# Kernel optimization log

Measured on AMD Instinct MI355X. Metric: run time of the kernel, lower is better.

The kernel has to match this reference:

```python
import jax, jax.numpy as jnp
import numpy as np

L = 8            # gat_blocks(4) * layers(2)
LAYERS = 2
RC, DC, SC, EC = 32, 32, 256, 512
IN_DIM, OUT_DIM = 2, 12
N_NODES, EMB, D_ATT = 512, 16, 16
B, T_IN = 8, 13  # T_IN == receptive_field -> no left padding


def setup_inputs() -> dict:
    key = jax.random.key(0)
    ks = jax.random.split(key, 12)
    g = lambda k, shp: jax.random.normal(k, shp, jnp.float32) * 0.05
    return {
        "input": jax.random.normal(ks[0], (B, IN_DIM, N_NODES, T_IN), jnp.float32),
        "gat_supports": jax.random.normal(ks[1], (EMB, N_NODES), jnp.float32),
        "start_w": g(ks[2], (RC, IN_DIM)), "start_b": jnp.zeros((RC,), jnp.float32),
        "filt_w": g(ks[3], (L, DC, RC, 1, 2)), "filt_b": jnp.zeros((L, DC), jnp.float32),
        "gate_w": g(ks[4], (L, DC, RC, 1, 2)), "gate_b": jnp.zeros((L, DC), jnp.float32),
        "skip_w": g(ks[5], (L, SC, DC)), "skip_b": jnp.zeros((L, SC), jnp.float32),
        "q_w": g(ks[6], (L, D_ATT, DC + EMB)), "q_b": jnp.zeros((L, D_ATT), jnp.float32),
        "k_w": g(ks[7], (L, D_ATT, DC + EMB)), "k_b": jnp.zeros((L, D_ATT), jnp.float32),
        "gmlp_w": g(ks[8], (L, RC, 2 * DC)), "gmlp_b": jnp.zeros((L, RC), jnp.float32),
        "bn_g": jnp.ones((L, RC), jnp.float32), "bn_b": jnp.zeros((L, RC), jnp.float32),
        "end1_w": g(ks[9], (EC, SC)), "end1_b": jnp.zeros((EC,), jnp.float32),
        "end2_w": g(ks[10], (OUT_DIM, EC)), "end2_b": jnp.zeros((OUT_DIM,), jnp.float32),
    }


def _pw(x, w, b):
    # 1x1 conv (pointwise linear over channels): x [B,C,N,T], w [O,C]
    return jnp.einsum('oc,bcnt->bont', w, x) + b[None, :, None, None]


def _tconv(x, w, b, d):
    # dilated temporal conv, kernel (1,2), VALID (shrinks T by d)
    y = jax.lax.conv_general_dilated(
        x, w, window_strides=(1, 1), padding='VALID', rhs_dilation=(1, d),
        dimension_numbers=('NCHW', 'OIHW', 'NCHW'))
    return y + b[None, :, None, None]


def _bn(x, g, b, eps=1e-5):
    # BatchNorm2d (training-mode batch stats, biased variance, as in torch)
    m = jnp.mean(x, axis=(0, 2, 3), keepdims=True)
    v = jnp.var(x, axis=(0, 2, 3), keepdims=True)
    return g[None, :, None, None] * (x - m) * jax.lax.rsqrt(v + eps) + b[None, :, None, None]


def _forward(input, gat_supports, start_w, start_b, filt_w, filt_b, gate_w, gate_b,
             skip_w, skip_b, q_w, q_b, k_w, k_b, gmlp_w, gmlp_b, bn_g, bn_b,
             end1_w, end1_b, end2_w, end2_b):
    x = _pw(input, start_w, start_b)          # [B,RC,N,T]
    skip = None
    scale = 1.0 / (D_ATT ** 0.5)
    for i in range(L):
        d = 2 ** (i % LAYERS)                 # dilation schedule 1,2 per block
        residual = x
        f = jnp.tanh(_tconv(residual, filt_w[i], filt_b[i], d))
        gt = jax.nn.sigmoid(_tconv(residual, gate_w[i], gate_b[i], d))
        x = f * gt                            # [B,DC,N,T-d]
        s = _pw(x, skip_w[i], skip_b[i])      # [B,SC,N,T-d]
        skip = s if skip is None else s + skip[:, :, :, -s.shape[3]:]
        # --- adaptive graph attention ---
        Bn, C, N, T = x.shape
        emb = jnp.broadcast_to(gat_supports[None, :, :, None], (Bn, EMB, N, T))
        xe = jnp.concatenate([x, emb], axis=1)            # [B,C+EMB,N,T]
        q = _pw(xe, q_w[i], q_b[i]).transpose(0, 3, 2, 1)  # [B,T,N,d]
        kk = _pw(xe, k_w[i], k_b[i]).transpose(0, 3, 2, 1)
        att = jax.nn.softmax(jnp.einsum('btnd,btmd->btnm', q, kk) * scale, axis=-1)
        xa = jnp.einsum('bcvt,btvw->bcwt', x, att)         # x @ att on node axis
        x = _pw(jnp.concatenate([x, xa], axis=1), gmlp_w[i], gmlp_b[i])
        # ---------------------------------
        x = x + residual[:, :, :, -x.shape[3]:]
        x = _bn(x, bn_g[i], bn_b[i])
    out = jax.nn.relu(skip)
    out = jax.nn.relu(_pw(out, end1_w, end1_b))
    out = _pw(out, end2_w, end2_b)            # [B,OUT_DIM,N,1]
    return out


def reference(input, gat_supports, start_w, start_b, filt_w, filt_b, gate_w, gate_b,
              skip_w, skip_b, q_w, q_b, k_w, k_b, gmlp_w, gmlp_b, bn_g, bn_b,
              end1_w, end1_b, end2_w, end2_b):
    return _forward(input, gat_supports, start_w, start_b, filt_w, filt_b, gate_w,
                    gate_b, skip_w, skip_b, q_w, q_b, k_w, k_b, gmlp_w, gmlp_b,
                    bn_g, bn_b, end1_w, end1_b, end2_w, end2_b)
```

## Files before the change

kernel.cpp:

```cpp
#include <hip/hip_runtime.h>
#include <math.h>


typedef short v4s __attribute__((ext_vector_type(4)));
typedef float v4f __attribute__((ext_vector_type(4)));
typedef unsigned short ushort_t;

#define MFMA16(a,b,c) __builtin_amdgcn_mfma_f32_16x16x16bf16_1k(a, b, c, 0, 0, 0)

__device__ inline ushort_t f2bf(float f){
    unsigned int u = __builtin_bit_cast(unsigned int, f);
    u += 0x7FFFu + ((u >> 16) & 1u);
    return (ushort_t)(u >> 16);
}
__device__ inline float bf2f(ushort_t h){
    return __builtin_bit_cast(float, ((unsigned int)h) << 16);
}

__global__ void k_init_norm(float* normP){
    int t = threadIdx.x;
    normP[t] = (t < 32) ? 1.0f : 0.0f;
}

__global__ void k_emb(const float* __restrict__ qw, const float* __restrict__ qb,
                      const float* __restrict__ kw, const float* __restrict__ kb,
                      const float* __restrict__ gat, float* __restrict__ qe, float* __restrict__ ke){
    int idx = blockIdx.x*256 + threadIdx.x;
    const int total = 8*512*16;
    if (idx >= 2*total) return;
    bool isK = idx >= total;
    int id = isK ? idx - total : idx;
    int dq = id & 15; int n = (id >> 4) & 511; int l = id >> 13;
    const float* w = isK ? kw : qw;
    const float* bi = isK ? kb : qb;
    float acc = bi[l*16 + dq];
    const float* wrow = w + (l*16 + dq)*48 + 32;
    #pragma unroll
    for (int e = 0; e < 16; e++) acc += wrow[e] * gat[e*512 + n];
    (isK ? ke : qe)[(l*512 + n)*16 + dq] = isK ? acc : acc*0.25f;
}

__global__ void k_start(const float* __restrict__ inp, const float* __restrict__ sw,
                        const float* __restrict__ sb, float* __restrict__ x0){
    int idx = blockIdx.x*256 + threadIdx.x;
    if (idx >= 8*13*32*512) return;
    int n = idx & 511; int c = (idx >> 9) & 31; int r = idx >> 14;
    int t = r % 13; int b = r / 13;
    float v0 = inp[((b*2 + 0)*512 + n)*13 + t];
    float v1 = inp[((b*2 + 1)*512 + n)*13 + t];
    x0[idx] = sb[c] + sw[c*2 + 0]*v0 + sw[c*2 + 1]*v1;
}

__global__ void k_wprep(const float* __restrict__ filt_w, const float* __restrict__ gate_w,
                        const float* __restrict__ q_w, const float* __restrict__ k_w,
                        const float* __restrict__ skip_w,
                        ushort_t* __restrict__ cwh, ushort_t* __restrict__ cwl,
                        ushort_t* __restrict__ qkw,
                        ushort_t* __restrict__ swh, ushort_t* __restrict__ swl)
{
    int idx = blockIdx.x*256 + threadIdx.x;
    if (idx < 32768){
        int k = idx & 63, o = (idx >> 6) & 63, l = idx >> 12;
        int c = k & 31, tap = k >> 5;
        float w = (o < 32) ? filt_w[((l*32 + o)*32 + c)*2 + tap]
                           : gate_w[((l*32 + (o-32))*32 + c)*2 + tap];
        ushort_t hi = f2bf(w);
        cwh[idx] = hi; cwl[idx] = f2bf(w - bf2f(hi));
    } else if (idx < 32768 + 8192){
        int j2 = idx - 32768;
        int c = j2 & 31, j = (j2 >> 5) & 31, l = j2 >> 10;
        float w = (j < 16) ? q_w[(l*16 + j)*48 + c]*0.25f : k_w[(l*16 + (j-16))*48 + c];
        qkw[j2] = f2bf(w);
    } else if (idx < 32768 + 8192 + 65536){
        int s = idx - 40960;
        float w = skip_w[s];
        ushort_t hi = f2bf(w);
        swh[s] = hi; swl[s] = f2bf(w - bf2f(hi));
    }
}

__global__ __launch_bounds__(256) void k_gated_mfma(
    const float* __restrict__ xin, int Tin, int d, int Tout,
    const float* __restrict__ normP,
    const ushort_t* __restrict__ cwh, const ushort_t* __restrict__ cwl,
    const float* __restrict__ fb, const float* __restrict__ gb,
    const ushort_t* __restrict__ qkw,
    const float* __restrict__ qe, const float* __restrict__ ke,
    const ushort_t* __restrict__ swh, const ushort_t* __restrict__ swl,
    const float* __restrict__ sb,
    float* __restrict__ skip,
    ushort_t* __restrict__ xbfT, ushort_t* __restrict__ qbf, ushort_t* __restrict__ kbf,
    int do_qk)
{
    __shared__ unsigned int XBP[64*129];
    int tid = threadIdx.x;
    int nch = blockIdx.x, t = blockIdx.y, b = blockIdx.z;
    size_t bt = (size_t)(b*Tout + t);
    int n0 = nch*128;
    int lane = tid & 63, wid = tid >> 6;
    int m16 = lane & 15, g4 = (lane >> 4)*4;

    #pragma unroll
    for (int kk = 0; kk < 16; kk++){
        int k = wid*16 + kk;
        int c = k & 31, tap = k >> 5;
        const float* src = xin + ((size_t)(b*Tin + t + tap*d)*32 + c)*512 + n0 + lane;
        float An = normP[c], Bn = normP[32 + c];
        #pragma unroll
        for (int h = 0; h < 2; h++){
            float xn = An*src[h*64] + Bn;
            ushort_t hi = f2bf(xn);
            ushort_t lo = f2bf(xn - bf2f(hi));
            XBP[k*129 + h*64 + lane] = (unsigned int)hi | ((unsigned int)lo << 16);
        }
    }
    v4s ah[4][4], al[4][4];
    #pragma unroll
    for (int ot = 0; ot < 4; ot++)
    #pragma unroll
    for (int kt = 0; kt < 4; kt++){
        ah[ot][kt] = *(const v4s*)(cwh + (ot*16 + m16)*64 + kt*16 + g4);
        al[ot][kt] = *(const v4s*)(cwl + (ot*16 + m16)*64 + kt*16 + g4);
    }
    v4f acc[4][2];
    #pragma unroll
    for (int ot = 0; ot < 4; ot++){
        float4 bv = *(const float4*)((ot < 2 ? fb + ot*16 : gb + (ot-2)*16) + g4);
        acc[ot][0] = (v4f){bv.x, bv.y, bv.z, bv.w};
        acc[ot][1] = (v4f){bv.x, bv.y, bv.z, bv.w};
    }
    __syncthreads();
    v4s bh[2][4], bl[2][4];
    #pragma unroll
    for (int nt = 0; nt < 2; nt++){
        int nl = (wid*2 + nt)*16 + m16;
        #pragma unroll
        for (int kt = 0; kt < 4; kt++){
            unsigned int u0 = XBP[(kt*16 + g4 + 0)*129 + nl];
            unsigned int u1 = XBP[(kt*16 + g4 + 1)*129 + nl];
            unsigned int u2 = XBP[(kt*16 + g4 + 2)*129 + nl];
            unsigned int u3 = XBP[(kt*16 + g4 + 3)*129 + nl];
            v4s hh, ll;
            hh[0] = (short)(u0 & 0xffffu); ll[0] = (short)(u0 >> 16);
            hh[1] = (short)(u1 & 0xffffu); ll[1] = (short)(u1 >> 16);
            hh[2] = (short)(u2 & 0xffffu); ll[2] = (short)(u2 >> 16);
            hh[3] = (short)(u3 & 0xffffu); ll[3] = (short)(u3 >> 16);
            bh[nt][kt] = hh; bl[nt][kt] = ll;
        }
    }
    #pragma unroll
    for (int kt = 0; kt < 4; kt++)
    #pragma unroll
    for (int ot = 0; ot < 4; ot++)
    #pragma unroll
    for (int nt = 0; nt < 2; nt++){
        acc[ot][nt] = MFMA16(ah[ot][kt], bh[nt][kt], acc[ot][nt]);
        acc[ot][nt] = MFMA16(ah[ot][kt], bl[nt][kt], acc[ot][nt]);
        acc[ot][nt] = MFMA16(al[ot][kt], bh[nt][kt], acc[ot][nt]);
    }
    v4s xh[2][2], xl[2][2];
    #pragma unroll
    for (int ct = 0; ct < 2; ct++)
    #pragma unroll
    for (int nt = 0; nt < 2; nt++){
        v4s hh, ll;
        #pragma unroll
        for (int i = 0; i < 4; i++){
            float f = acc[ct][nt][i], g = acc[ct+2][nt][i];
            float e2 = __expf(2.0f*f);
            float th = 1.0f - 2.0f/(e2 + 1.0f);
            float sg = 1.0f/(1.0f + __expf(-g));
            float v = th*sg;
            ushort_t hi = f2bf(v);
            hh[i] = (short)hi; ll[i] = (short)f2bf(v - bf2f(hi));
        }
        xh[ct][nt] = hh; xl[ct][nt] = ll;
    }
    if (do_qk){
        #pragma unroll
        for (int ct = 0; ct < 2; ct++)
        #pragma unroll
        for (int nt = 0; nt < 2; nt++){
            int nl = n0 + (wid*2 + nt)*16 + m16;
            #pragma unroll
            for (int i = 0; i < 4; i++)
                xbfT[(bt*32 + ct*16 + g4 + i)*512 + nl] = (ushort_t)xh[ct][nt][i];
        }
        v4s qa[2][2];
        #pragma unroll
        for (int ot = 0; ot < 2; ot++)
        #pragma unroll
        for (int kt = 0; kt < 2; kt++)
            qa[ot][kt] = *(const v4s*)(qkw + (ot*16 + m16)*32 + kt*16 + g4);
        #pragma unroll
        for (int ot = 0; ot < 2; ot++)
        #pragma unroll
        for (int nt = 0; nt < 2; nt++){
            int nl = n0 + (wid*2 + nt)*16 + m16;
            float4 ev = *(const float4*)((ot == 0 ? qe : ke) + nl*16 + g4);
            v4f a2 = (v4f){ev.x, ev.y, ev.z, ev.w};
            #pragma unroll
            for (int kt = 0; kt < 2; kt++)
                a2 = MFMA16(qa[ot][kt], xh[kt][nt], a2);
            v4s r;
            #pragma unroll
            for (int i = 0; i < 4; i++) r[i] = (short)f2bf(a2[i]);
            *(v4s*)((ot == 0 ? qbf : kbf) + (bt*512 + nl)*16 + g4) = r;
        }
    }
    if (t == Tout - 1){
        #pragma unroll 4
        for (int ot = 0; ot < 16; ot++){
            v4s sh_[2], sl_[2];
            #pragma unroll
            for (int kt = 0; kt < 2; kt++){
                sh_[kt] = *(const v4s*)(swh + (ot*16 + m16)*32 + kt*16 + g4);
                sl_[kt] = *(const v4s*)(swl + (ot*16 + m16)*32 + kt*16 + g4);
            }
            float4 sbv = *(const float4*)(sb + ot*16 + g4);
            #pragma unroll
            for (int nt = 0; nt < 2; nt++){
                int nl = n0 + (wid*2 + nt)*16 + m16;
                float* sp = skip + ((size_t)(b*512) + nl)*256 + ot*16 + g4;
                float4 old = *(const float4*)sp;
                v4f a3 = (v4f){old.x + sbv.x, old.y + sbv.y, old.z + sbv.z, old.w + sbv.w};
                #pragma unroll
                for (int kt = 0; kt < 2; kt++){
                    a3 = MFMA16(sh_[kt], xh[kt][nt], a3);
                    a3 = MFMA16(sh_[kt], xl[kt][nt], a3);
                    a3 = MFMA16(sl_[kt], xh[kt][nt], a3);
                }
                *(float4*)sp = make_float4(a3[0], a3[1], a3[2], a3[3]);
            }
        }
    }
}

__global__ __launch_bounds__(256) void k_z(
    const ushort_t* __restrict__ qbf, const ushort_t* __restrict__ kbf,
    int Tout, float* __restrict__ rz)
{
    __shared__ ushort_t KS[512*20];
    int tid = threadIdx.x;
    int vchunk = blockIdx.x, t = blockIdx.y, b = blockIdx.z;
    size_t bt = (size_t)(b*Tout + t);
    const ushort_t* kg = kbf + bt*8192;
    const ushort_t* qg = qbf + bt*8192;
    {
        const uint2* s0 = (const uint2*)(kg + tid*16);
        uint2* d0 = (uint2*)(KS + tid*20);
        d0[0]=s0[0]; d0[1]=s0[1]; d0[2]=s0[2]; d0[3]=s0[3];
        const uint2* s1 = (const uint2*)(kg + (tid+256)*16);
        uint2* d1 = (uint2*)(KS + (tid+256)*20);
        d1[0]=s1[0]; d1[1]=s1[1]; d1[2]=s1[2]; d1[3]=s1[3];
    }
    int l = tid & 63, wid = tid >> 6;
    int m16 = l & 15, g4 = (l >> 4)*4;
    __syncthreads();
    #pragma unroll
    for (int vi = 0; vi < 2; vi++){
        int vt = vchunk*8 + wid*2 + vi;
        v4s bq = *(const v4s*)(qg + (vt*16 + m16)*16 + g4);
        float zp = 0.f;
        for (int wt = 0; wt < 32; wt++){
            v4s ak = *(const v4s*)(KS + (wt*16 + m16)*20 + g4);
            v4f s = MFMA16(ak, bq, ((v4f){0.f,0.f,0.f,0.f}));
            zp += __expf(fminf(s[0],60.f)) + __expf(fminf(s[1],60.f))
                + __expf(fminf(s[2],60.f)) + __expf(fminf(s[3],60.f));
        }
        zp += __shfl_xor(zp, 16);
        zp += __shfl_xor(zp, 32);
        if (l < 16) rz[bt*512 + vt*16 + l] = 1.0f/zp;
    }
}

__global__ __launch_bounds__(256) void k_pv(
    const ushort_t* __restrict__ qbf, const ushort_t* __restrict__ kbf,
    const ushort_t* __restrict__ xbfT, const float* __restrict__ rz,
    const float* __restrict__ xin, int Tin, int d, int Tout,
    const float* __restrict__ normP,
    const float* __restrict__ gw, const float* __restrict__ gb,
    float* __restrict__ y, float* __restrict__ bnpart)
{
    __shared__ ushort_t QS[512*20];
    __shared__ ushort_t XT[32*520];
    __shared__ float rzs[512];
    __shared__ float bnsh[256];
    int tid = threadIdx.x;
    int wc = blockIdx.x, t = blockIdx.y, b = blockIdx.z;
    size_t bt = (size_t)(b*Tout + t);
    const ushort_t* qg = qbf + bt*8192;
    const ushort_t* kg = kbf + bt*8192;
    {
        const uint2* s0 = (const uint2*)(qg + tid*16);
        uint2* d0 = (uint2*)(QS + tid*20);
        d0[0]=s0[0]; d0[1]=s0[1]; d0[2]=s0[2]; d0[3]=s0[3];
        const uint2* s1 = (const uint2*)(qg + (tid+256)*16);
        uint2* d1 = (uint2*)(QS + (tid+256)*20);
        d1[0]=s1[0]; d1[1]=s1[1]; d1[2]=s1[2]; d1[3]=s1[3];
        int c = tid >> 3, seg = tid & 7;
        const uint4* xs = (const uint4*)(xbfT + bt*16384 + c*512 + seg*64);
        uint4* xd = (uint4*)(XT + c*520 + seg*64);
        #pragma unroll
        for (int j = 0; j < 8; j++) xd[j] = xs[j];
        rzs[tid] = rz[bt*512 + tid];
        rzs[tid + 256] = rz[bt*512 + tid + 256];
    }
    int l = tid & 63, wid = tid >> 6;
    int m16 = l & 15, g4 = (l >> 4)*4;
    v4s AG[2][2][2];
    #pragma unroll
    for (int pt = 0; pt < 2; pt++)
    #pragma unroll
    for (int ot = 0; ot < 2; ot++)
    #pragma unroll
    for (int ct = 0; ct < 2; ct++){
        float4 gv = *(const float4*)(gw + (ot*16 + m16)*64 + pt*32 + ct*16 + g4);
        v4s r; r[0] = (short)f2bf(gv.x); r[1] = (short)f2bf(gv.y);
        r[2] = (short)f2bf(gv.z); r[3] = (short)f2bf(gv.w);
        AG[pt][ot][ct] = r;
    }
    v4f gbv[2], An[2], Bn[2];
    #pragma unroll
    for (int ot = 0; ot < 2; ot++){
        gbv[ot] = *(const v4f*)(gb + ot*16 + g4);
        An[ot]  = *(const v4f*)(normP + ot*16 + g4);
        Bn[ot]  = *(const v4f*)(normP + 32 + ot*16 + g4);
    }
    int wt0 = wc*8 + wid*2;
    v4s bk[2];
    bk[0] = *(const v4s*)(kg + (wt0*16 + m16)*16 + g4);
    bk[1] = *(const v4s*)(kg + ((wt0+1)*16 + m16)*16 + g4);
    __syncthreads();
    v4f c2[2][2];
    #pragma unroll
    for (int i = 0; i < 2; i++){ c2[i][0] = (v4f){0.f,0.f,0.f,0.f}; c2[i][1] = (v4f){0.f,0.f,0.f,0.f}; }
    for (int vt = 0; vt < 32; vt++){
        v4s aq = *(const v4s*)(QS + (vt*16 + m16)*20 + g4);
        v4f s0 = MFMA16(aq, bk[0], ((v4f){0.f,0.f,0.f,0.f}));
        v4f s1 = MFMA16(aq, bk[1], ((v4f){0.f,0.f,0.f,0.f}));
        v4f rzv = *(const v4f*)(rzs + vt*16 + g4);
        v4s p0, p1;
        #pragma unroll
        for (int i = 0; i < 4; i++){
            p0[i] = (short)f2bf(__expf(fminf(s0[i],60.f)) * rzv[i]);
            p1[i] = (short)f2bf(__expf(fminf(s1[i],60.f)) * rzv[i]);
        }
        #pragma unroll
        for (int ct = 0; ct < 2; ct++){
            v4s ax = *(const v4s*)(XT + (ct*16 + m16)*520 + vt*16 + g4);
            c2[0][ct] = MFMA16(ax, p0, c2[0][ct]);
            c2[1][ct] = MFMA16(ax, p1, c2[1][ct]);
        }
    }
    float bs1[2][4], bs2[2][4];
    #pragma unroll
    for (int ot = 0; ot < 2; ot++)
    #pragma unroll
    for (int i = 0; i < 4; i++){ bs1[ot][i] = 0.f; bs2[ot][i] = 0.f; }
    #pragma unroll
    for (int wtl = 0; wtl < 2; wtl++){
        int wt = wt0 + wtl;
        v4s bxa[2], bx[2];
        #pragma unroll
        for (int ct = 0; ct < 2; ct++){
            v4s r;
            #pragma unroll
            for (int i = 0; i < 4; i++) r[i] = (short)f2bf(c2[wtl][ct][i]);
            bxa[ct] = r;
            v4s q;
            #pragma unroll
            for (int i = 0; i < 4; i++) q[i] = (short)XT[(ct*16 + g4 + i)*520 + wt*16 + m16];
            bx[ct] = q;
        }
        v4f c3[2];
        #pragma unroll
        for (int ot = 0; ot < 2; ot++){
            c3[ot] = gbv[ot];
            #pragma unroll
            for (int ct = 0; ct < 2; ct++){
                c3[ot] = MFMA16(AG[1][ot][ct], bxa[ct], c3[ot]);
                c3[ot] = MFMA16(AG[0][ot][ct], bx[ct],  c3[ot]);
            }
        }
        int wg = wt*16 + m16;
        const float* resbase = xin + ((size_t)(b*Tin + t + d)*32)*512 + wg;
        float* ybase = y + (bt*32)*512 + wg;
        #pragma unroll
        for (int ot = 0; ot < 2; ot++){
            #pragma unroll
            for (int i = 0; i < 4; i++){
                int outc = ot*16 + g4 + i;
                float yv = c3[ot][i] + An[ot][i]*resbase[(size_t)outc*512] + Bn[ot][i];
                ybase[(size_t)outc*512] = yv;
                bs1[ot][i] += yv; bs2[ot][i] += yv*yv;
            }
        }
    }
    #pragma unroll
    for (int off = 1; off <= 8; off <<= 1){
        #pragma unroll
        for (int ot = 0; ot < 2; ot++)
        #pragma unroll
        for (int i = 0; i < 4; i++){
            bs1[ot][i] += __shfl_xor(bs1[ot][i], off);
            bs2[ot][i] += __shfl_xor(bs2[ot][i], off);
        }
    }
    if (m16 == 0){
        #pragma unroll
        for (int ot = 0; ot < 2; ot++)
        #pragma unroll
        for (int i = 0; i < 4; i++){
            int c = ot*16 + g4 + i;
            bnsh[(wid*32 + c)*2 + 0] = bs1[ot][i];
            bnsh[(wid*32 + c)*2 + 1] = bs2[ot][i];
        }
    }
    __syncthreads();
    if (tid < 64){
        int c = tid & 31, p = tid >> 5;
        float s = 0.f;
        #pragma unroll
        for (int w = 0; w < 4; w++) s += bnsh[(w*32 + c)*2 + p];
        bnpart[(bt*4 + wc)*64 + c*2 + p] = s;
    }
}

__global__ __launch_bounds__(1024) void k_bn_fin(
    const float* __restrict__ bnpart, int nparts,
    const float* __restrict__ g, const float* __restrict__ bb,
    float* __restrict__ normPout)
{
    __shared__ float sh[17][64];
    int tid = threadIdx.x;
    int lane = tid & 63, grp = tid >> 6;
    float s = 0.f;
    for (int i = grp; i < nparts; i += 16) s += bnpart[(size_t)i*64 + lane];
    sh[grp][lane] = s;
    __syncthreads();
    if (tid < 64){
        float tot = 0.f;
        #pragma unroll
        for (int gg = 0; gg < 16; gg++) tot += sh[gg][lane];
        sh[16][lane] = tot;
    }
    __syncthreads();
    if (tid < 32){
        float S  = sh[16][tid*2 + 0];
        float S2 = sh[16][tid*2 + 1];
        float cnt = (float)nparts * 128.0f;
        float m = S/cnt;
        float var = S2/cnt - m*m;
        float A = g[tid]*rsqrtf(var + 1e-5f);
        normPout[tid] = A;
        normPout[32 + tid] = bb[tid] - m*A;
    }
}

__global__ void k_split_skip(const float* __restrict__ skip,
                             ushort_t* __restrict__ shi, ushort_t* __restrict__ slo){
    int idx = blockIdx.x*256 + threadIdx.x;
    float v = fmaxf(skip[idx], 0.f);
    ushort_t h = f2bf(v);
    shi[idx] = h; slo[idx] = f2bf(v - bf2f(h));
}

__global__ void k_w1split(const float* __restrict__ w,
                          ushort_t* __restrict__ hi, ushort_t* __restrict__ lo){
    int idx = blockIdx.x*256 + threadIdx.x;
    float v = w[idx];
    ushort_t h = f2bf(v);
    hi[idx] = h; lo[idx] = f2bf(v - bf2f(h));
}

__global__ __launch_bounds__(256) void k_end_h(
    const ushort_t* __restrict__ shi, const ushort_t* __restrict__ slo,
    const ushort_t* __restrict__ w1hi, const ushort_t* __restrict__ w1lo,
    const float* __restrict__ b1, float* __restrict__ h)
{
    __shared__ ushort_t SH[16*264], SL[16*264];
    int tid = threadIdx.x;
    int nc = blockIdx.x, b = blockIdx.y;
    int n0 = nc*16;
    {
        int n = tid >> 4, s = tid & 15;
        const uint4* src = (const uint4*)(shi + ((size_t)(b*512 + n0 + n))*256 + s*16);
        uint4* dst = (uint4*)(SH + n*264 + s*16);
        dst[0] = src[0]; dst[1] = src[1];
        const uint4* src2 = (const uint4*)(slo + ((size_t)(b*512 + n0 + n))*256 + s*16);
        uint4* dst2 = (uint4*)(SL + n*264 + s*16);
        dst2[0] = src2[0]; dst2[1] = src2[1];
    }
    __syncthreads();
    int l = tid & 63, wid = tid >> 6;
    int m16 = l & 15, g4 = (l >> 4)*4;
    v4f acc[8];
    #pragma unroll
    for (int nt = 0; nt < 8; nt++){
        float bo = b1[(wid*8 + nt)*16 + m16];
        acc[nt] = (v4f){bo, bo, bo, bo};
    }
    for (int kk = 0; kk < 16; kk++){
        v4s ahi = *(const v4s*)(SH + m16*264 + kk*16 + g4);
        v4s alo = *(const v4s*)(SL + m16*264 + kk*16 + g4);
        #pragma unroll
        for (int nt = 0; nt < 8; nt++){
            int o = (wid*8 + nt)*16 + m16;
            v4s bhi = *(const v4s*)(w1hi + o*256 + kk*16 + g4);
            v4s blo = *(const v4s*)(w1lo + o*256 + kk*16 + g4);
            acc[nt] = MFMA16(ahi, bhi, acc[nt]);
            acc[nt] = MFMA16(ahi, blo, acc[nt]);
            acc[nt] = MFMA16(alo, bhi, acc[nt]);
        }
    }
    #pragma unroll
    for (int nt = 0; nt < 8; nt++){
        int o = (wid*8 + nt)*16 + m16;
        float4 hv;
        hv.x = fmaxf(acc[nt][0], 0.f);
        hv.y = fmaxf(acc[nt][1], 0.f);
        hv.z = fmaxf(acc[nt][2], 0.f);
        hv.w = fmaxf(acc[nt][3], 0.f);
        *(float4*)(h + ((size_t)(b*512 + o))*512 + n0 + g4) = hv;
    }
}

__global__ __launch_bounds__(64) void k_end2(
    const float* __restrict__ h, const float* __restrict__ w2, const float* __restrict__ b2,
    float* __restrict__ out)
{
    int l = threadIdx.x;
    int nc = blockIdx.x, b = blockIdx.y;
    int n = nc*16 + (l & 15);
    int grp = l >> 4;
    float a0 = b2[grp], a1 = b2[grp+4], a2 = b2[grp+8];
    const float* hb = h + ((size_t)b*512)*512 + n;
    const float* w0 = w2 + (size_t)grp*512;
    const float* w4 = w2 + (size_t)(grp+4)*512;
    const float* w8 = w2 + (size_t)(grp+8)*512;
    for (int o = 0; o < 512; o++){
        float hv = hb[(size_t)o*512];
        a0 += w0[o]*hv; a1 += w4[o]*hv; a2 += w8[o]*hv;
    }
    out[((size_t)b*12 + grp)*512 + n] = a0;
    out[((size_t)b*12 + grp+4)*512 + n] = a1;
    out[((size_t)b*12 + grp+8)*512 + n] = a2;
}

extern "C" void kernel_launch(void* const* d_in, const int* in_sizes, int n_in,
                              void* d_out, int out_size, void* d_ws, size_t ws_size,
                              hipStream_t stream)
{
    (void)in_sizes; (void)n_in; (void)out_size; (void)ws_size;
    const float* input  = (const float*)d_in[0];
    const float* gat    = (const float*)d_in[1];
    const float* start_w= (const float*)d_in[2];
    const float* start_b= (const float*)d_in[3];
    const float* filt_w = (const float*)d_in[4];
    const float* filt_b = (const float*)d_in[5];
    const float* gate_w = (const float*)d_in[6];
    const float* gate_b = (const float*)d_in[7];
    const float* skip_w = (const float*)d_in[8];
    const float* skip_b = (const float*)d_in[9];
    const float* q_w    = (const float*)d_in[10];
    const float* q_b    = (const float*)d_in[11];
    const float* k_w    = (const float*)d_in[12];
    const float* k_b    = (const float*)d_in[13];
    const float* gmlp_w = (const float*)d_in[14];
    const float* gmlp_b = (const float*)d_in[15];
    const float* bn_g   = (const float*)d_in[16];
    const float* bn_b   = (const float*)d_in[17];
    const float* end1_w = (const float*)d_in[18];
    const float* end1_b = (const float*)d_in[19];
    const float* end2_w = (const float*)d_in[20];
    const float* end2_b = (const float*)d_in[21];
    float* out = (float*)d_out;

    float* W = (float*)d_ws;
    size_t off = 0;
    float* bufA = W + off; off += (size_t)8*13*32*512;
    float* bufB = W + off; off += (size_t)8*13*32*512;
    float* skip = W + off; off += (size_t)8*512*256;
    float* qe   = W + off; off += (size_t)8*512*16;
    float* ke   = W + off; off += (size_t)8*512*16;
    float* normP= W + off; off += (size_t)9*64;
    float* bnpart = W + off; off += (size_t)96*4*64;
    float* rz   = W + off; off += (size_t)8*12*512;
    float* h    = W + off; off += (size_t)8*512*512;
    ushort_t* xbfT = (ushort_t*)(W + off); off += (size_t)8*12*32*512/2;
    ushort_t* qbf  = (ushort_t*)(W + off); off += (size_t)8*12*512*16/2;
    ushort_t* kbf  = (ushort_t*)(W + off); off += (size_t)8*12*512*16/2;
    ushort_t* shi  = (ushort_t*)(W + off); off += (size_t)8*512*256/2;
    ushort_t* slo  = (ushort_t*)(W + off); off += (size_t)8*512*256/2;
    ushort_t* w1hi = (ushort_t*)(W + off); off += (size_t)512*256/2;
    ushort_t* w1lo = (ushort_t*)(W + off); off += (size_t)512*256/2;
    ushort_t* cwh  = (ushort_t*)(W + off); off += (size_t)32768/2;
    ushort_t* cwl  = (ushort_t*)(W + off); off += (size_t)32768/2;
    ushort_t* qkw  = (ushort_t*)(W + off); off += (size_t)8192/2;
    ushort_t* swbh = (ushort_t*)(W + off); off += (size_t)65536/2;
    ushort_t* swbl = (ushort_t*)(W + off); off += (size_t)65536/2;

    hipMemsetAsync(skip, 0, (size_t)8*512*256*sizeof(float), stream);
    k_init_norm<<<1, 64, 0, stream>>>(normP);
    k_emb<<<512, 256, 0, stream>>>(q_w, q_b, k_w, k_b, gat, qe, ke);
    k_start<<<6656, 256, 0, stream>>>(input, start_w, start_b, bufA);
    k_w1split<<<512, 256, 0, stream>>>(end1_w, w1hi, w1lo);
    k_wprep<<<416, 256, 0, stream>>>(filt_w, gate_w, q_w, k_w, skip_w, cwh, cwl, qkw, swbh, swbl);

    const int Tin[8] = {13,12,10,9,7,6,4,3};
    const int Dd[8]  = {1,2,1,2,1,2,1,2};
    float* xin = bufA; float* yb = bufB;
    for (int i = 0; i < 8; i++){
        int Ti = Tin[i], d = Dd[i], To = Ti - d;
        k_gated_mfma<<<dim3(4, To, 8), 256, 0, stream>>>(xin, Ti, d, To, normP + i*64,
            cwh + i*4096, cwl + i*4096, filt_b + i*32, gate_b + i*32,
            qkw + i*1024, qe + i*8192, ke + i*8192,
            swbh + i*8192, swbl + i*8192, skip_b + i*256,
            skip, xbfT, qbf, kbf, (i < 7) ? 1 : 0);
        if (i < 7){
            k_z<<<dim3(4, To, 8), 256, 0, stream>>>(qbf, kbf, To, rz);
            k_pv<<<dim3(4, To, 8), 256, 0, stream>>>(qbf, kbf, xbfT, rz,
                xin, Ti, d, To, normP + i*64, gmlp_w + i*2048, gmlp_b + i*32, yb, bnpart);
            k_bn_fin<<<1, 1024, 0, stream>>>(bnpart, 8*To*4, bn_g + i*32, bn_b + i*32, normP + (i+1)*64);
            float* tmp = xin; xin = yb; yb = tmp;
        }
    }
    k_split_skip<<<4096, 256, 0, stream>>>(skip, shi, slo);
    k_end_h<<<dim3(32, 8), 256, 0, stream>>>(shi, slo, w1hi, w1lo, end1_b, h);
    k_end2<<<dim3(32, 8), 64, 0, stream>>>(h, end2_w, end2_b, out);
}
```

Baseline: 501.1 us.

## Fold BN finalize into consumers via atomics and fuse end layers into one kernel

Drops the separate batch-norm finalize kernel: k_pv now atomically accumulates per-channel sums, and the next-layer kernels turn them into scale and shift themselves. Fuses skip ReLU and bf16 splitting, end1 and end2 into a single kernel, with end2 done on MFMA using LDS-resident hidden activations. Also merges the end1 and end2 weight prep into k_wprep and removes the init-norm launch. This cuts kernel launches and the global round trips for h, shi and slo, at the cost of atomic contention and a non-deterministic summation order for the BN statistics.

```diff
diff --git a/kernel.cpp b/kernel.cpp
--- a/kernel.cpp
+++ b/kernel.cpp
@@ -15,11 +15,6 @@
 }
 __device__ inline float bf2f(ushort_t h){
     return __builtin_bit_cast(float, ((unsigned int)h) << 16);
-}
-
-__global__ void k_init_norm(float* normP){
-    int t = threadIdx.x;
-    normP[t] = (t < 32) ? 1.0f : 0.0f;
 }
 
 __global__ void k_emb(const float* __restrict__ qw, const float* __restrict__ qb,
@@ -54,9 +49,12 @@
 __global__ void k_wprep(const float* __restrict__ filt_w, const float* __restrict__ gate_w,
                         const float* __restrict__ q_w, const float* __restrict__ k_w,
                         const float* __restrict__ skip_w,
+                        const float* __restrict__ w1, const float* __restrict__ w2,
                         ushort_t* __restrict__ cwh, ushort_t* __restrict__ cwl,
                         ushort_t* __restrict__ qkw,
-                        ushort_t* __restrict__ swh, ushort_t* __restrict__ swl)
+                        ushort_t* __restrict__ swh, ushort_t* __restrict__ swl,
+                        ushort_t* __restrict__ w1h, ushort_t* __restrict__ w1l,
+                        ushort_t* __restrict__ w2h, ushort_t* __restrict__ w2l)
 {
     int idx = blockIdx.x*256 + threadIdx.x;
     if (idx < 32768){
@@ -66,22 +64,34 @@
                            : gate_w[((l*32 + (o-32))*32 + c)*2 + tap];
         ushort_t hi = f2bf(w);
         cwh[idx] = hi; cwl[idx] = f2bf(w - bf2f(hi));
-    } else if (idx < 32768 + 8192){
+    } else if (idx < 40960){
         int j2 = idx - 32768;
         int c = j2 & 31, j = (j2 >> 5) & 31, l = j2 >> 10;
         float w = (j < 16) ? q_w[(l*16 + j)*48 + c]*0.25f : k_w[(l*16 + (j-16))*48 + c];
         qkw[j2] = f2bf(w);
-    } else if (idx < 32768 + 8192 + 65536){
+    } else if (idx < 106496){
         int s = idx - 40960;
         float w = skip_w[s];
         ushort_t hi = f2bf(w);
         swh[s] = hi; swl[s] = f2bf(w - bf2f(hi));
+    } else if (idx < 237568){
+        int s = idx - 106496;
+        float w = w1[s];
+        ushort_t hi = f2bf(w);
+        w1h[s] = hi; w1l[s] = f2bf(w - bf2f(hi));
+    } else if (idx < 245760){
+        int s = idx - 237568;
+        int od = s >> 9, k = s & 511;
+        float w = (od < 12) ? w2[od*512 + k] : 0.0f;
+        ushort_t hi = f2bf(w);
+        w2h[s] = hi; w2l[s] = f2bf(w - bf2f(hi));
     }
 }
 
 __global__ __launch_bounds__(256) void k_gated_mfma(
     const float* __restrict__ xin, int Tin, int d, int Tout,
-    const float* __restrict__ normP,
+    const float* __restrict__ bnsumP, const float* __restrict__ bnG,
+    const float* __restrict__ bnB, int ident, float cnt,
     const ushort_t* __restrict__ cwh, const ushort_t* __restrict__ cwl,
     const float* __restrict__ fb, const float* __restrict__ gb,
     const ushort_t* __restrict__ qkw,
@@ -93,6 +103,7 @@
     int do_qk)
 {
     __shared__ unsigned int XBP[64*129];
+    __shared__ float ABsh[64];
     int tid = threadIdx.x;
     int nch = blockIdx.x, t = blockIdx.y, b = blockIdx.z;
     size_t bt = (size_t)(b*Tout + t);
@@ -100,12 +111,25 @@
     int lane = tid & 63, wid = tid >> 6;
     int m16 = lane & 15, g4 = (lane >> 4)*4;
 
+    if (tid < 32){
+        float A, Bc;
+        if (ident){ A = 1.0f; Bc = 0.0f; }
+        else {
+            float S = bnsumP[2*tid], S2 = bnsumP[2*tid + 1];
+            float m = S/cnt, var = S2/cnt - m*m;
+            A = bnG[tid]*rsqrtf(var + 1e-5f);
+            Bc = bnB[tid] - m*A;
+        }
+        ABsh[tid] = A; ABsh[32 + tid] = Bc;
+    }
+    __syncthreads();
+
     #pragma unroll
     for (int kk = 0; kk < 16; kk++){
         int k = wid*16 + kk;
         int c = k & 31, tap = k >> 5;
         const float* src = xin + ((size_t)(b*Tin + t + tap*d)*32 + c)*512 + n0 + lane;
-        float An = normP[c], Bn = normP[32 + c];
+        float An = ABsh[c], Bn = ABsh[32 + c];
         #pragma unroll
         for (int h = 0; h < 2; h++){
             float xn = An*src[h*64] + Bn;
@@ -278,14 +302,16 @@
     const ushort_t* __restrict__ qbf, const ushort_t* __restrict__ kbf,
     const ushort_t* __restrict__ xbfT, const float* __restrict__ rz,
     const float* __restrict__ xin, int Tin, int d, int Tout,
-    const float* __restrict__ normP,
+    const float* __restrict__ bnsumP, const float* __restrict__ bnG,
+    const float* __restrict__ bnB, int ident, float cnt,
     const float* __restrict__ gw, const float* __restrict__ gb,
-    float* __restrict__ y, float* __restrict__ bnpart)
+    float* __restrict__ y, float* __restrict__ bnsumOut)
 {
     __shared__ ushort_t QS[512*20];
     __shared__ ushort_t XT[32*520];
     __shared__ float rzs[512];
     __shared__ float bnsh[256];
+    __shared__ float ABsh[64];
     int tid = threadIdx.x;
     int wc = blockIdx.x, t = blockIdx.y, b = blockIdx.z;
     size_t bt = (size_t)(b*Tout + t);
@@ -306,6 +332,17 @@
         rzs[tid] = rz[bt*512 + tid];
         rzs[tid + 256] = rz[bt*512 + tid + 256];
     }
+    if (tid < 32){
+        float A, Bc;
+        if (ident){ A = 1.0f; Bc = 0.0f; }
+        else {
+            float S = bnsumP[2*tid], S2 = bnsumP[2*tid + 1];
+            float m = S/cnt, var = S2/cnt - m*m;
+            A = bnG[tid]*rsqrtf(var + 1e-5f);
+            Bc = bnB[tid] - m*A;
+        }
+        ABsh[tid] = A; ABsh[32 + tid] = Bc;
+    }
     int l = tid & 63, wid = tid >> 6;
     int m16 = l & 15, g4 = (l >> 4)*4;
     v4s AG[2][2][2];
@@ -320,18 +357,23 @@
         r[2] = (short)f2bf(gv.z); r[3] = (short)f2bf(gv.w);
         AG[pt][ot][ct] = r;
     }
-    v4f gbv[2], An[2], Bn[2];
-    #pragma unroll
-    for (int ot = 0; ot < 2; ot++){
-        gbv[ot] = *(const v4f*)(gb + ot*16 + g4);
-        An[ot]  = *(const v4f*)(normP + ot*16 + g4);
-        Bn[ot]  = *(const v4f*)(normP + 32 + ot*16 + g4);
-    }
+    v4f gbv[2];
+    #pragma unroll
+    for (int ot = 0; ot < 2; ot++) gbv[ot] = *(const v4f*)(gb + ot*16 + g4);
     int wt0 = wc*8 + wid*2;
     v4s bk[2];
     bk[0] = *(const v4s*)(kg + (wt0*16 + m16)*16 + g4);
     bk[1] = *(const v4s*)(kg + ((wt0+1)*16 + m16)*16 + g4);
     __syncthreads();
+    v4f An[2], Bn[2];
+    #pragma unroll
+    for (int ot = 0; ot < 2; ot++){
+        #pragma unroll
+        for (int i = 0; i < 4; i++){
+            An[ot][i] = ABsh[ot*16 + g4 + i];
+            Bn[ot][i] = ABsh[32 + ot*16 + g4 + i];
+        }
+    }
     v4f c2[2][2];
     #pragma unroll
     for (int i = 0; i < 2; i++){ c2[i][0] = (v4f){0.f,0.f,0.f,0.f}; c2[i][1] = (v4f){0.f,0.f,0.f,0.f}; }
@@ -423,74 +465,37 @@
         float s = 0.f;
         #pragma unroll
         for (int w = 0; w < 4; w++) s += bnsh[(w*32 + c)*2 + p];
-        bnpart[(bt*4 + wc)*64 + c*2 + p] = s;
-    }
-}
-
-__global__ __launch_bounds__(1024) void k_bn_fin(
-    const float* __restrict__ bnpart, int nparts,
-    const float* __restrict__ g, const float* __restrict__ bb,
-    float* __restrict__ normPout)
-{
-    __shared__ float sh[17][64];
-    int tid = threadIdx.x;
-    int lane = tid & 63, grp = tid >> 6;
-    float s = 0.f;
-    for (int i = grp; i < nparts; i += 16) s += bnpart[(size_t)i*64 + lane];
-    sh[grp][lane] = s;
-    __syncthreads();
-    if (tid < 64){
-        float tot = 0.f;
-        #pragma unroll
-        for (int gg = 0; gg < 16; gg++) tot += sh[gg][lane];
-        sh[16][lane] = tot;
-    }
-    __syncthreads();
-    if (tid < 32){
-        float S  = sh[16][tid*2 + 0];
-        float S2 = sh[16][tid*2 + 1];
-        float cnt = (float)nparts * 128.0f;
-        float m = S/cnt;
-        float var = S2/cnt - m*m;
-        float A = g[tid]*rsqrtf(var + 1e-5f);
-        normPout[tid] = A;
-        normPout[32 + tid] = bb[tid] - m*A;
-    }
-}
-
-__global__ void k_split_skip(const float* __restrict__ skip,
-                             ushort_t* __restrict__ shi, ushort_t* __restrict__ slo){
-    int idx = blockIdx.x*256 + threadIdx.x;
-    float v = fmaxf(skip[idx], 0.f);
-    ushort_t h = f2bf(v);
-    shi[idx] = h; slo[idx] = f2bf(v - bf2f(h));
-}
-
-__global__ void k_w1split(const float* __restrict__ w,
-                          ushort_t* __restrict__ hi, ushort_t* __restrict__ lo){
-    int idx = blockIdx.x*256 + threadIdx.x;
-    float v = w[idx];
-    ushort_t h = f2bf(v);
-    hi[idx] = h; lo[idx] = f2bf(v - bf2f(h));
-}
-
-__global__ __launch_bounds__(256) void k_end_h(
-    const ushort_t* __restrict__ shi, const ushort_t* __restrict__ slo,
+        atomicAdd(&bnsumOut[c*2 + p], s);
+    }
+}
+
+__global__ __launch_bounds__(256) void k_end_all(
+    const float* __restrict__ skip,
     const ushort_t* __restrict__ w1hi, const ushort_t* __restrict__ w1lo,
-    const float* __restrict__ b1, float* __restrict__ h)
+    const float* __restrict__ b1,
+    const ushort_t* __restrict__ w2hi, const ushort_t* __restrict__ w2lo,
+    const float* __restrict__ b2, float* __restrict__ out)
 {
     __shared__ ushort_t SH[16*264], SL[16*264];
+    __shared__ ushort_t HH[512*17], HL[512*17];
     int tid = threadIdx.x;
     int nc = blockIdx.x, b = blockIdx.y;
     int n0 = nc*16;
     {
         int n = tid >> 4, s = tid & 15;
-        const uint4* src = (const uint4*)(shi + ((size_t)(b*512 + n0 + n))*256 + s*16);
-        uint4* dst = (uint4*)(SH + n*264 + s*16);
-        dst[0] = src[0]; dst[1] = src[1];
-        const uint4* src2 = (const uint4*)(slo + ((size_t)(b*512 + n0 + n))*256 + s*16);
-        uint4* dst2 = (uint4*)(SL + n*264 + s*16);
-        dst2[0] = src2[0]; dst2[1] = src2[1];
+        const float4* src = (const float4*)(skip + ((size_t)(b*512 + n0 + n))*256 + s*16);
+        #pragma unroll
+        for (int j = 0; j < 4; j++){
+            float4 v4_ = src[j];
+            float vv[4] = {v4_.x, v4_.y, v4_.z, v4_.w};
+            #pragma unroll
+            for (int e = 0; e < 4; e++){
+                float v = fmaxf(vv[e], 0.f);
+                ushort_t h = f2bf(v);
+                SH[n*264 + s*16 + j*4 + e] = h;
+                SL[n*264 + s*16 + j*4 + e] = f2bf(v - bf2f(h));
+            }
+        }
     }
     __syncthreads();
     int l = tid & 63, wid = tid >> 6;
@@ -517,35 +522,43 @@
     #pragma unroll
     for (int nt = 0; nt < 8; nt++){
         int o = (wid*8 + nt)*16 + m16;
-        float4 hv;
-        hv.x = fmaxf(acc[nt][0], 0.f);
-        hv.y = fmaxf(acc[nt][1], 0.f);
-        hv.z = fmaxf(acc[nt][2], 0.f);
-        hv.w = fmaxf(acc[nt][3], 0.f);
-        *(float4*)(h + ((size_t)(b*512 + o))*512 + n0 + g4) = hv;
-    }
-}
-
-__global__ __launch_bounds__(64) void k_end2(
-    const float* __restrict__ h, const float* __restrict__ w2, const float* __restrict__ b2,
-    float* __restrict__ out)
-{
-    int l = threadIdx.x;
-    int nc = blockIdx.x, b = blockIdx.y;
-    int n = nc*16 + (l & 15);
-    int grp = l >> 4;
-    float a0 = b2[grp], a1 = b2[grp+4], a2 = b2[grp+8];
-    const float* hb = h + ((size_t)b*512)*512 + n;
-    const float* w0 = w2 + (size_t)grp*512;
-    const float* w4 = w2 + (size_t)(grp+4)*512;
-    const float* w8 = w2 + (size_t)(grp+8)*512;
-    for (int o = 0; o < 512; o++){
-        float hv = hb[(size_t)o*512];
-        a0 += w0[o]*hv; a1 += w4[o]*hv; a2 += w8[o]*hv;
-    }
-    out[((size_t)b*12 + grp)*512 + n] = a0;
-    out[((size_t)b*12 + grp+4)*512 + n] = a1;
-    out[((size_t)b*12 + grp+8)*512 + n] = a2;
+        #pragma unroll
+        for (int i = 0; i < 4; i++){
+            float v = fmaxf(acc[nt][i], 0.f);
+            ushort_t h = f2bf(v);
+            HH[o*17 + g4 + i] = h;
+            HL[o*17 + g4 + i] = f2bf(v - bf2f(h));
+        }
+    }
+    __syncthreads();
+    if (wid == 0){
+        v4f a4;
+        #pragma unroll
+        for (int i = 0; i < 4; i++){
+            int od = g4 + i;
+            a4[i] = (od < 12) ? b2[od] : 0.f;
+        }
+        for (int kt = 0; kt < 32; kt++){
+            v4s wh, wl, hh, hl;
+            #pragma unroll
+            for (int i = 0; i < 4; i++){
+                int k = kt*16 + g4 + i;
+                wh[i] = (short)w2hi[m16*512 + k];
+                wl[i] = (short)w2lo[m16*512 + k];
+                hh[i] = (short)HH[k*17 + m16];
+                hl[i] = (short)HL[k*17 + m16];
+            }
+            a4 = MFMA16(wh, hh, a4);
+            a4 = MFMA16(wh, hl, a4);
+            a4 = MFMA16(wl, hh, a4);
+        }
+        #pragma unroll
+        for (int i = 0; i < 4; i++){
+            int od = g4 + i;
+            if (od < 12)
+                out[((size_t)(b*12 + od))*512 + n0 + m16] = a4[i];
+        }
+    }
 }
 
 extern "C" void kernel_launch(void* const* d_in, const int* in_sizes, int n_in,
@@ -579,41 +592,44 @@
 
     float* W = (float*)d_ws;
     size_t off = 0;
+    float* skip = W + off; off += (size_t)8*512*256;
+    float* bnsum= W + off; off += (size_t)7*64;
     float* bufA = W + off; off += (size_t)8*13*32*512;
     float* bufB = W + off; off += (size_t)8*13*32*512;
-    float* skip = W + off; off += (size_t)8*512*256;
     float* qe   = W + off; off += (size_t)8*512*16;
     float* ke   = W + off; off += (size_t)8*512*16;
-    float* normP= W + off; off += (size_t)9*64;
-    float* bnpart = W + off; off += (size_t)96*4*64;
     float* rz   = W + off; off += (size_t)8*12*512;
-    float* h    = W + off; off += (size_t)8*512*512;
     ushort_t* xbfT = (ushort_t*)(W + off); off += (size_t)8*12*32*512/2;
     ushort_t* qbf  = (ushort_t*)(W + off); off += (size_t)8*12*512*16/2;
     ushort_t* kbf  = (ushort_t*)(W + off); off += (size_t)8*12*512*16/2;
-    ushort_t* shi  = (ushort_t*)(W + off); off += (size_t)8*512*256/2;
-    ushort_t* slo  = (ushort_t*)(W + off); off += (size_t)8*512*256/2;
-    ushort_t* w1hi = (ushort_t*)(W + off); off += (size_t)512*256/2;
-    ushort_t* w1lo = (ushort_t*)(W + off); off += (size_t)512*256/2;
     ushort_t* cwh  = (ushort_t*)(W + off); off += (size_t)32768/2;
     ushort_t* cwl  = (ushort_t*)(W + off); off += (size_t)32768/2;
     ushort_t* qkw  = (ushort_t*)(W + off); off += (size_t)8192/2;
     ushort_t* swbh = (ushort_t*)(W + off); off += (size_t)65536/2;
     ushort_t* swbl = (ushort_t*)(W + off); off += (size_t)65536/2;
-
-    hipMemsetAsync(skip, 0, (size_t)8*512*256*sizeof(float), stream);
-    k_init_norm<<<1, 64, 0, stream>>>(normP);
+    ushort_t* w1hi = (ushort_t*)(W + off); off += (size_t)512*256/2;
+    ushort_t* w1lo = (ushort_t*)(W + off); off += (size_t)512*256/2;
+    ushort_t* w2hi = (ushort_t*)(W + off); off += (size_t)16*512/2;
+    ushort_t* w2lo = (ushort_t*)(W + off); off += (size_t)16*512/2;
+
+    hipMemsetAsync(skip, 0, ((size_t)8*512*256 + 7*64)*sizeof(float), stream);
     k_emb<<<512, 256, 0, stream>>>(q_w, q_b, k_w, k_b, gat, qe, ke);
     k_start<<<6656, 256, 0, stream>>>(input, start_w, start_b, bufA);
-    k_w1split<<<512, 256, 0, stream>>>(end1_w, w1hi, w1lo);
-    k_wprep<<<416, 256, 0, stream>>>(filt_w, gate_w, q_w, k_w, skip_w, cwh, cwl, qkw, swbh, swbl);
+    k_wprep<<<960, 256, 0, stream>>>(filt_w, gate_w, q_w, k_w, skip_w, end1_w, end2_w,
+                                     cwh, cwl, qkw, swbh, swbl, w1hi, w1lo, w2hi, w2lo);
 
     const int Tin[8] = {13,12,10,9,7,6,4,3};
     const int Dd[8]  = {1,2,1,2,1,2,1,2};
     float* xin = bufA; float* yb = bufB;
     for (int i = 0; i < 8; i++){
         int Ti = Tin[i], d = Dd[i], To = Ti - d;
-        k_gated_mfma<<<dim3(4, To, 8), 256, 0, stream>>>(xin, Ti, d, To, normP + i*64,
+        const float* bnsumP = (i == 0) ? bnsum : bnsum + (i-1)*64;
+        const float* gP = (i == 0) ? bn_g : bn_g + (i-1)*32;
+        const float* bP = (i == 0) ? bn_b : bn_b + (i-1)*32;
+        int ident = (i == 0) ? 1 : 0;
+        float cnt = 8.0f * (float)Ti * 512.0f;
+        k_gated_mfma<<<dim3(4, To, 8), 256, 0, stream>>>(xin, Ti, d, To,
+            bnsumP, gP, bP, ident, cnt,
             cwh + i*4096, cwl + i*4096, filt_b + i*32, gate_b + i*32,
             qkw + i*1024, qe + i*8192, ke + i*8192,
             swbh + i*8192, swbl + i*8192, skip_b + i*256,
@@ -621,12 +637,10 @@
         if (i < 7){
             k_z<<<dim3(4, To, 8), 256, 0, stream>>>(qbf, kbf, To, rz);
             k_pv<<<dim3(4, To, 8), 256, 0, stream>>>(qbf, kbf, xbfT, rz,
-                xin, Ti, d, To, normP + i*64, gmlp_w + i*2048, gmlp_b + i*32, yb, bnpart);
-            k_bn_fin<<<1, 1024, 0, stream>>>(bnpart, 8*To*4, bn_g + i*32, bn_b + i*32, normP + (i+1)*64);
+                xin, Ti, d, To, bnsumP, gP, bP, ident, cnt,
+                gmlp_w + i*2048, gmlp_b + i*32, yb, bnsum + i*64);
             float* tmp = xin; xin = yb; yb = tmp;
         }
     }
-    k_split_skip<<<4096, 256, 0, stream>>>(skip, shi, slo);
-    k_end_h<<<dim3(32, 8), 256, 0, stream>>>(shi, slo, w1hi, w1lo, end1_b, h);
-    k_end2<<<dim3(32, 8), 64, 0, stream>>>(h, end2_w, end2_b, out);
-}
+    k_end_all<<<dim3(32, 8), 256, 0, stream>>>(skip, w1hi, w1lo, end1_b, w2hi, w2lo, end2_b, out);
+}
```

Measured after the change: 449.6 us. -10.3%, faster.
